# Optimization experiments

Hardware: AMD Instinct MI355X
Metric: run time of the kernel (lower is better)

## Reference

```python
import jax, jax.numpy as jnp
import numpy as np

B, S, D, H, T = 64, 512, 768, 384, 22  # batch, seq, bert dim, lstm hidden, tagset+2


def setup_inputs() -> dict:
    key = jax.random.key(0)
    ks = jax.random.split(key, 14)
    hidden_states = jax.random.normal(ks[0], (B, S, D), jnp.float32)
    # strictly increasing wordpiece start offsets, -1 padded (per-sample variable length)
    nw = np.array([S // 2 - (b % 16) * 4 for b in range(B)])  # number of valid start ids
    sid = -np.ones((B, S), np.int64)
    msk = np.zeros((B, S), np.int64)
    for b in range(B):
        sid[b, : nw[b]] = 1 + 2 * np.arange(nw[b])  # max = 2*nw-1 <= S-1
        msk[b, : nw[b] + 1] = 1  # word-level mask: nw+1 words incl. CLS slot
    start_ids = jnp.asarray(sid)
    masks = jnp.asarray(msk)
    sc = 0.05
    h0 = jax.random.normal(ks[1], (2, B, H), jnp.float32)
    c0 = jax.random.normal(ks[2], (2, B, H), jnp.float32)
    W_ih_f = jax.random.normal(ks[3], (4 * H, D), jnp.float32) * sc
    W_hh_f = jax.random.normal(ks[4], (4 * H, H), jnp.float32) * sc
    b_ih_f = jax.random.normal(ks[5], (4 * H,), jnp.float32) * sc
    b_hh_f = jax.random.normal(ks[6], (4 * H,), jnp.float32) * sc
    W_ih_b = jax.random.normal(ks[7], (4 * H, D), jnp.float32) * sc
    W_hh_b = jax.random.normal(ks[8], (4 * H, H), jnp.float32) * sc
    b_ih_b = jax.random.normal(ks[9], (4 * H,), jnp.float32) * sc
    b_hh_b = jax.random.normal(ks[10], (4 * H,), jnp.float32) * sc
    W_lin = jax.random.normal(ks[11], (T, 2 * H), jnp.float32) * sc
    b_lin = jax.random.normal(ks[12], (T,), jnp.float32) * sc
    return {"hidden_states": hidden_states, "h0": h0, "c0": c0,
            "W_ih_f": W_ih_f, "W_hh_f": W_hh_f, "b_ih_f": b_ih_f, "b_hh_f": b_hh_f,
            "W_ih_b": W_ih_b, "W_hh_b": W_hh_b, "b_ih_b": b_ih_b, "b_hh_b": b_hh_b,
            "W_lin": W_lin, "b_lin": b_lin, "start_ids": start_ids, "masks": masks}


def _lstm_dir(x, h0, c0, Wih, Whh, bih, bhh, reverse):
    # x: [B,S,D]; torch gate order i,f,g,o
    xg = jnp.einsum('bsd,gd->bsg', x, Wih) + bih + bhh  # [B,S,4H]
    xs = jnp.swapaxes(xg, 0, 1)  # [S,B,4H]
    if reverse:
        xs = xs[::-1]

    def step(carry, xt):
        h, c = carry
        g = xt + h @ Whh.T
        i, f, gg, o = jnp.split(g, 4, axis=-1)
        c = jax.nn.sigmoid(f) * c + jax.nn.sigmoid(i) * jnp.tanh(gg)
        h = jax.nn.sigmoid(o) * jnp.tanh(c)
        return (h, c), h

    _, hs = jax.lax.scan(step, (h0, c0), xs)
    if reverse:
        hs = hs[::-1]
    return jnp.swapaxes(hs, 0, 1)  # [B,S,H]


def _align(hidden_states, start_ids, masks):
    # word t embedding: t==0 -> token 0 (CLS); 1<=t<n -> token start_ids[t]-1
    # (last wordpiece of word t); t==n -> token start_ids[n-1]; else zero-pad.
    Bb, Ss, _ = hidden_states.shape
    t = jnp.arange(Ss)[None, :]
    valid = start_ids >= 0
    n = valid.sum(-1)  # [B] number of valid start ids
    last_sid = jnp.take_along_axis(start_ids, (n - 1)[:, None], axis=1)  # [B,1]
    idx = jnp.where(t == 0, 0,
          jnp.where(t < n[:, None], start_ids - 1,
          jnp.where(t == n[:, None], last_sid, 0)))
    idx = jnp.clip(idx, 0, Ss - 1)
    gathered = jnp.take_along_axis(hidden_states, idx[:, :, None], axis=1)
    sent_len = masks.sum(-1)  # word-level lengths (second loop in torch code)
    keep = (t < sent_len[:, None])[:, :, None]
    return jnp.where(keep, gathered, 0.0)


def reference(hidden_states, h0, c0, W_ih_f, W_hh_f, b_ih_f, b_hh_f,
              W_ih_b, W_hh_b, b_ih_b, b_hh_b, W_lin, b_lin, start_ids, masks):
    embeds = _align(hidden_states, start_ids, masks)  # q=1,k=0 => wordpiece-only
    hf = _lstm_dir(embeds, h0[0], c0[0], W_ih_f, W_hh_f, b_ih_f, b_hh_f, False)
    hb = _lstm_dir(embeds, h0[1], c0[1], W_ih_b, W_hh_b, b_ih_b, b_hh_b, True)
    lstm_out = jnp.concatenate([hf, hb], axis=-1)  # [B,S,2H]
    # dropout1 is identity in eval mode
    feats = lstm_out @ W_lin.T + b_lin  # [B,S,T]
    return feats
```

## Files before the change

### kernel.cpp

```cpp
#include <hip/hip_runtime.h>

typedef unsigned short u16;
typedef unsigned int u32;
typedef unsigned long long u64;

typedef short bf16x8 __attribute__((ext_vector_type(8)));
typedef float f32x4 __attribute__((ext_vector_type(4)));

#define NB 64
#define NS 512
#define ND 768
#define NH 384
#define NT_OUT 22
#define S2 272
#define NG 1536
#define MGEMM (NB*S2)

__device__ __forceinline__ u16 f2b(float f) {
    u32 u = __float_as_uint(f);
    u32 r = (u + 0x7fffu + ((u >> 16) & 1u)) >> 16;
    return (u16)r;
}
__device__ __forceinline__ float b2f(u16 s) { return __uint_as_float(((u32)s) << 16); }

__device__ __forceinline__ float sigm(float x) {
    return __builtin_amdgcn_rcpf(1.f + __expf(-x));
}
__device__ __forceinline__ float tanh_(float x) {
    return 1.f - 2.f * __builtin_amdgcn_rcpf(1.f + __expf(2.f * x));
}

__device__ __forceinline__ void gl_lds16(const void* g, void* l) {
    __builtin_amdgcn_global_load_lds(
        (const __attribute__((address_space(1))) unsigned int*)g,
        (__attribute__((address_space(3))) unsigned int*)l, 16, 0, 0);
}

__global__ void k_prep(const float* __restrict__ hidden, const int* __restrict__ start_ids,
                       const int* __restrict__ masks, u16* __restrict__ embeds) {
    int b = blockIdx.x >> 2;
    int quarter = blockIdx.x & 3;
    int tid = threadIdx.x;
    __shared__ int red[256];
    int cn = 0, cm = 0;
    for (int s = tid; s < NS; s += 256) {
        cn += (start_ids[b * NS + s] >= 0) ? 1 : 0;
        cm += (masks[b * NS + s] != 0) ? 1 : 0;
    }
    red[tid] = cn + (cm << 16);
    __syncthreads();
    #pragma unroll
    for (int off = 128; off > 0; off >>= 1) {
        if (tid < off) red[tid] += red[tid + off];
        __syncthreads();
    }
    int n = red[0] & 0xffff;
    int slen = red[0] >> 16;
    n = min(max(n, 1), NS);
    int last = start_ids[b * NS + n - 1];
    for (int t = quarter * 68; t < quarter * 68 + 68; ++t) {
        int idx;
        if (t == 0) idx = 0;
        else if (t < n) idx = start_ids[b * NS + t] - 1;
        else if (t == n) idx = last;
        else idx = 0;
        idx = min(max(idx, 0), NS - 1);
        bool keep = t < slen;
        const float* src = hidden + ((size_t)b * NS + idx) * ND;
        u16* dst = embeds + ((size_t)b * S2 + t) * ND;
        if (tid < 192) {
            float4 v = keep ? *(const float4*)(src + tid * 4) : make_float4(0.f, 0.f, 0.f, 0.f);
            union { u16 u[4]; uint2 q; } pk;
            pk.u[0] = f2b(v.x); pk.u[1] = f2b(v.y); pk.u[2] = f2b(v.z); pk.u[3] = f2b(v.w);
            *(uint2*)(dst + tid * 4) = pk.q;
        }
    }
}

__global__ void k_weights(const float* __restrict__ wf, const float* __restrict__ wb,
                          const float* __restrict__ bihf, const float* __restrict__ bhhf,
                          const float* __restrict__ bihb, const float* __restrict__ bhhb,
                          const float* __restrict__ h0,
                          u16* __restrict__ wihcat, float* __restrict__ biascat,
                          u16* __restrict__ h0buf) {
    int i0 = blockIdx.x * blockDim.x + threadIdx.x;
    int NTH = gridDim.x * blockDim.x;
    for (size_t i = i0; i < (size_t)2 * NG * ND; i += NTH) {
        size_t nrow = i / ND, k = i - nrow * ND;
        float v = (nrow < NG) ? wf[nrow * ND + k] : wb[(nrow - NG) * ND + k];
        wihcat[i] = f2b(v);
    }
    for (int i = i0; i < 2 * NG; i += NTH)
        biascat[i] = (i < NG) ? bihf[i] + bhhf[i] : bihb[i - NG] + bhhb[i - NG];
    for (int i = i0; i < 2 * NB * NH; i += NTH) h0buf[i] = f2b(h0[i]);
}

__global__ void k_packwhh(const float* __restrict__ whhf, const float* __restrict__ whhb,
                          u16* __restrict__ pack) {
    int ft = blockIdx.x * 256 + threadIdx.x;
    if (ft >= 2 * 4 * 4 * 6 * 12 * 64) return;
    int lane = ft & 63;
    int grp = ft >> 6;
    int ks = grp % 12; grp /= 12;
    int nt = grp % 6;  grp /= 6;
    int w  = grp & 3;  grp >>= 2;
    int qc = grp & 3;
    int d  = grp >> 2;
    const float* W = d ? whhb : whhf;
    int col = w * NH + qc * 96 + nt * 16 + (lane & 15);
    int k0 = ks * 32 + (lane >> 4) * 8;
    u16* dst = pack + (size_t)ft * 8;
    #pragma unroll
    for (int e = 0; e < 8; e++) dst[e] = f2b(W[(size_t)col * NH + k0 + e]);
}

__launch_bounds__(256, 2)
__global__ void k_gemm(const u16* __restrict__ A, const u16* __restrict__ Bw,
                       const float* __restrict__ biascat, u16* __restrict__ xg) {
    __shared__ u16 As[128 * 32];
    __shared__ u16 Bs[128 * 32];
    int tid = threadIdx.x;
    int lane = tid & 63, wid = tid >> 6;
    int l15 = lane & 15, q4 = lane >> 4;
    int bn = blockIdx.x;
    int bm = blockIdx.y;
    int wm = (wid >> 1) * 64, wn = (wid & 1) * 64;
    f32x4 acc[4][4] = {};
    for (int k0 = 0; k0 < ND; k0 += 32) {
        #pragma unroll
        for (int j = 0; j < 2; j++) {
            int fl = tid + j * 256;
            int row = fl >> 2, cb = fl & 3;
            const u16* ga = A + (size_t)(bm * 128 + row) * ND + k0 + cb * 8;
            gl_lds16(ga, &As[(size_t)(wid * 64 + j * 256) * 8]);
            const u16* gb = Bw + (size_t)(bn * 128 + row) * ND + k0 + cb * 8;
            gl_lds16(gb, &Bs[(size_t)(wid * 64 + j * 256) * 8]);
        }
        __syncthreads();
        bf16x8 af[4], bf[4];
        #pragma unroll
        for (int mt = 0; mt < 4; mt++)
            af[mt] = *(const bf16x8*)&As[(wm + mt * 16 + l15) * 32 + q4 * 8];
        #pragma unroll
        for (int nt = 0; nt < 4; nt++)
            bf[nt] = *(const bf16x8*)&Bs[(wn + nt * 16 + l15) * 32 + q4 * 8];
        #pragma unroll
        for (int mt = 0; mt < 4; mt++)
            #pragma unroll
            for (int nt = 0; nt < 4; nt++)
                acc[mt][nt] = __builtin_amdgcn_mfma_f32_16x16x32_bf16(af[mt], bf[nt], acc[mt][nt], 0, 0, 0);
        __syncthreads();
    }
    #pragma unroll
    for (int nt = 0; nt < 4; nt++) {
        int gn = bn * 128 + wn + nt * 16 + l15;
        int d = gn >= NG ? 1 : 0;
        int col = gn - d * NG;
        float bias = biascat[gn];
        #pragma unroll
        for (int mt = 0; mt < 4; mt++) {
            #pragma unroll
            for (int r = 0; r < 4; r++) {
                int m = bm * 128 + wm + mt * 16 + q4 * 4 + r;
                int b = m / S2, t = m - b * S2;
                float v = acc[mt][nt][r] + bias;
                xg[((size_t)(d * NB + b) * S2 + t) * NG + col] = f2b(v);
            }
        }
    }
}

__launch_bounds__(256, 1)
__global__ void k_recur(const u16* __restrict__ whhpack, const u16* __restrict__ xg,
                        const float* __restrict__ biascat, const u16* __restrict__ h0buf,
                        const float* __restrict__ c0, u16* __restrict__ hout,
                        int* __restrict__ flags) {
    int blk = blockIdx.x;
    int qc = blk >> 3;
    int cl = blk & 7;
    int d = cl >> 2;
    int g = cl & 3;
    int tid = threadIdx.x, lane = tid & 63, w = tid >> 6;
    int q4 = lane >> 4, l15 = lane & 15;

    __shared__ float preact[4][16 * 96];

    bf16x8 bfr[6][12];
    #pragma unroll
    for (int nt = 0; nt < 6; nt++)
        #pragma unroll
        for (int ks = 0; ks < 12; ks++)
            bfr[nt][ks] = *(const bf16x8*)(whhpack +
                ((size_t)((((d * 4 + qc) * 4 + w) * 6 + nt) * 12 + ks) * 64 + lane) * 8);

    int bb = tid / 12;
    int j0 = (tid % 12) * 8;
    float cre[8];
    if (tid < 192) {
        const float* cp = c0 + (size_t)(d * NB + g * 16 + bb) * NH + qc * 96 + j0;
        #pragma unroll
        for (int e = 0; e < 8; e++) cre[e] = cp[e];
    }
    float biasreg[6];
    #pragma unroll
    for (int nt = 0; nt < 6; nt++)
        biasreg[nt] = biascat[d * NG + w * NH + qc * 96 + nt * 16 + l15];

    int* flagp = flags + cl * NS;
    const u16* hd = hout + (size_t)d * NB * NS * NH;
    const u16* xgd = xg + (size_t)d * NB * S2 * NG;

    float ci[6][4];
    auto preload = [&](int it2) {
        int s2 = d ? (NS - 1 - it2) : it2;
        if (s2 < S2) {
            const u16* xrow = xgd + ((size_t)(g * 16) * S2 + s2) * NG + w * NH + qc * 96 + l15;
            #pragma unroll
            for (int nt = 0; nt < 6; nt++)
                #pragma unroll
                for (int r = 0; r < 4; r++)
                    ci[nt][r] = b2f(xrow[(size_t)(q4 * 4 + r) * S2 * NG + nt * 16]);
        } else {
            #pragma unroll
            for (int nt = 0; nt < 6; nt++)
                #pragma unroll
                for (int r = 0; r < 4; r++) ci[nt][r] = biasreg[nt];
        }
    };
    preload(0);

    int dep = 0;
    #pragma unroll 1
    for (int it = 0; it < NS; ++it) {
        int s = d ? (NS - 1 - it) : it;
        int tprev = d ? (s + 1) : (s - 1);

        bf16x8 af[12];
        if (it == 0) {
            const u16* hp = h0buf + (size_t)(d * NB + g * 16) * NH;
            #pragma unroll
            for (int ks = 0; ks < 12; ks++)
                af[ks] = *(const bf16x8*)(hp + (size_t)l15 * NH + ks * 32 + q4 * 8);
        } else {
            const u64* hp = (const u64*)(hd + ((size_t)(g * 16) * NS + tprev) * NH) + dep;
            #pragma unroll
            for (int ks = 0; ks < 12; ks++) {
                union { u64 q[2]; bf16x8 v; } u;
                const u64* p = hp + ((size_t)l15 * NS * NH + (size_t)ks * 32 + q4 * 8) / 4;
                u.q[0] = __hip_atomic_load(p,     __ATOMIC_RELAXED, __HIP_MEMORY_SCOPE_AGENT);
                u.q[1] = __hip_atomic_load(p + 1, __ATOMIC_RELAXED, __HIP_MEMORY_SCOPE_AGENT);
                af[ks] = u.v;
            }
        }

        f32x4 acc[6];
        #pragma unroll
        for (int nt = 0; nt < 6; nt++) {
            acc[nt][0] = ci[nt][0]; acc[nt][1] = ci[nt][1];
            acc[nt][2] = ci[nt][2]; acc[nt][3] = ci[nt][3];
        }
        #pragma unroll
        for (int ks = 0; ks < 12; ks++)
            #pragma unroll
            for (int nt = 0; nt < 6; nt++)
                acc[nt] = __builtin_amdgcn_mfma_f32_16x16x32_bf16(af[ks], bfr[nt][ks], acc[nt], 0, 0, 0);

        #pragma unroll
        for (int nt = 0; nt < 6; nt++)
            #pragma unroll
            for (int r = 0; r < 4; r++)
                preact[w][(q4 * 4 + r) * 96 + nt * 16 + l15] = acc[nt][r];
        __syncthreads();

        if (tid < 192) {
            int idx = bb * 96 + j0;
            u16* ho = hout + (((size_t)(d * NB + g * 16 + bb)) * NS + s) * NH + qc * 96 + j0;
            union { u16 u[8]; u64 q[2]; } pk;
            #pragma unroll
            for (int e = 0; e < 8; e++) {
                float gi = preact[0][idx + e], gf = preact[1][idx + e];
                float gg = preact[2][idx + e], go = preact[3][idx + e];
                float c = cre[e];
                float cn = sigm(gf) * c + sigm(gi) * tanh_(gg);
                float hn = sigm(go) * tanh_(cn);
                cre[e] = cn;
                pk.u[e] = f2b(hn);
            }
            __hip_atomic_store((u64*)ho,     pk.q[0], __ATOMIC_RELAXED, __HIP_MEMORY_SCOPE_AGENT);
            __hip_atomic_store((u64*)ho + 1, pk.q[1], __ATOMIC_RELAXED, __HIP_MEMORY_SCOPE_AGENT);
        }
        __syncthreads();

        if (tid == 0)
            __hip_atomic_fetch_add(&flagp[it], 1, __ATOMIC_RELAXED, __HIP_MEMORY_SCOPE_AGENT);

        if (it == NS - 1) break;

        preload(it + 1);

        int fv = 4;
        if (lane == 0) {
            while ((fv = __hip_atomic_load(&flagp[it], __ATOMIC_RELAXED, __HIP_MEMORY_SCOPE_AGENT)) < 4)
                __builtin_amdgcn_s_sleep(1);
        }
        fv = __shfl(fv, 0);
        dep = fv - 4;
    }
}

__global__ void k_final(const u16* __restrict__ hout, const float* __restrict__ wlin,
                        const float* __restrict__ blin, float* __restrict__ out) {
    int r = blockIdx.x * 256 + threadIdx.x;
    int b = r >> 9, t = r & 511;
    const u16* hf = hout + ((size_t)b * NS + t) * NH;
    const u16* hb = hout + ((size_t)(NB + b) * NS + t) * NH;
    float acc[NT_OUT];
    #pragma unroll
    for (int tt = 0; tt < NT_OUT; tt++) acc[tt] = blin[tt];
    #pragma unroll 1
    for (int half = 0; half < 2; half++) {
        const u16* hp = half ? hb : hf;
        #pragma unroll 1
        for (int k8 = 0; k8 < NH / 8; k8++) {
            uint4 pk = *(const uint4*)(hp + k8 * 8);
            float x[8];
            x[0] = __uint_as_float(pk.x << 16); x[1] = __uint_as_float(pk.x & 0xffff0000u);
            x[2] = __uint_as_float(pk.y << 16); x[3] = __uint_as_float(pk.y & 0xffff0000u);
            x[4] = __uint_as_float(pk.z << 16); x[5] = __uint_as_float(pk.z & 0xffff0000u);
            x[6] = __uint_as_float(pk.w << 16); x[7] = __uint_as_float(pk.w & 0xffff0000u);
            int kk = half * NH + k8 * 8;
            #pragma unroll
            for (int e = 0; e < 8; e++)
                #pragma unroll
                for (int tt = 0; tt < NT_OUT; tt++)
                    acc[tt] += x[e] * wlin[tt * (2 * NH) + kk + e];
        }
    }
    float* op = out + (size_t)r * NT_OUT;
    #pragma unroll
    for (int tt = 0; tt < NT_OUT; tt++) op[tt] = acc[tt];
}

extern "C" void kernel_launch(void* const* d_in, const int* in_sizes, int n_in,
                              void* d_out, int out_size, void* d_ws, size_t ws_size,
                              hipStream_t stream) {
    const float* hidden = (const float*)d_in[0];
    const float* h0     = (const float*)d_in[1];
    const float* c0     = (const float*)d_in[2];
    const float* Wihf   = (const float*)d_in[3];
    const float* Whhf   = (const float*)d_in[4];
    const float* bihf   = (const float*)d_in[5];
    const float* bhhf   = (const float*)d_in[6];
    const float* Wihb   = (const float*)d_in[7];
    const float* Whhb   = (const float*)d_in[8];
    const float* bihb   = (const float*)d_in[9];
    const float* bhhb   = (const float*)d_in[10];
    const float* Wlin   = (const float*)d_in[11];
    const float* blin   = (const float*)d_in[12];
    const int* start_ids = (const int*)d_in[13];
    const int* masks     = (const int*)d_in[14];
    float* out = (float*)d_out;

    char* ws = (char*)d_ws;
    size_t off = 0;
    auto alloc = [&](size_t bytes) { void* p = ws + off; off += (bytes + 255) & ~(size_t)255; return p; };
    u16* embeds   = (u16*)alloc((size_t)MGEMM * ND * 2);
    u16* wihcat   = (u16*)alloc((size_t)2 * NG * ND * 2);
    float* biascat = (float*)alloc((size_t)2 * NG * 4);
    u16* whhpack  = (u16*)alloc((size_t)2 * NG * NH * 2);
    u16* h0buf    = (u16*)alloc((size_t)2 * NB * NH * 2);
    u16* xg       = (u16*)alloc((size_t)2 * NB * S2 * NG * 2);
    u16* hout     = (u16*)alloc((size_t)2 * NB * NS * NH * 2);
    int* flags    = (int*)alloc((size_t)8 * NS * 4);

    (void)hipMemsetAsync(flags, 0, (size_t)8 * NS * 4, stream);
    k_prep<<<256, 256, 0, stream>>>(hidden, start_ids, masks, embeds);
    k_weights<<<512, 256, 0, stream>>>(Wihf, Wihb, bihf, bhhf, bihb, bhhb, h0,
                                       wihcat, biascat, h0buf);
    k_packwhh<<<576, 256, 0, stream>>>(Whhf, Whhb, whhpack);
    dim3 ggrid(2 * NG / 128, MGEMM / 128);
    k_gemm<<<ggrid, 256, 0, stream>>>(embeds, wihcat, biascat, xg);
    k_recur<<<32, 256, 0, stream>>>(whhpack, xg, biascat, h0buf, c0, hout, flags);
    k_final<<<128, 256, 0, stream>>>(hout, Wlin, blin, out);
}
```

Baseline: 3.051 ms.

## Replace per-step flag barrier with tagged h-exchange buffer and staggered partial MFMAs

The recurrence kernel no longer publishes h to the large hout array and then spins on a per-step counter flag. Each of the four cooperating blocks now writes its 96-column slice of h into a small triple-buffered exchange array, with the step number tagged into the low 16 bits of each word. Consumers poll those words directly, checking a sum of tags, and start MFMAs on their own slice (kept in LDS) before the peers' slices arrive, so the K loop is rotated per block. A startup handshake tests whether all four blocks of a cluster can see each other's writes with sc0 (non-coherent-L2-bypass) accesses and falls back to sc0 sc1 otherwise. This is meant to remove the flag round trip and the full barrier from the serial critical path, at the cost of inline asm cache-policy tricks and extra polling traffic.

```diff
diff --git a/kernel.cpp b/kernel.cpp
--- a/kernel.cpp
+++ b/kernel.cpp
@@ -6,6 +6,7 @@
 
 typedef short bf16x8 __attribute__((ext_vector_type(8)));
 typedef float f32x4 __attribute__((ext_vector_type(4)));
+typedef u32 u32x4 __attribute__((ext_vector_type(4)));
 
 #define NB 64
 #define NS 512
@@ -15,6 +16,7 @@
 #define S2 272
 #define NG 1536
 #define MGEMM (NB*S2)
+#define MAGIC 0x5A5AA5A5u
 
 __device__ __forceinline__ u16 f2b(float f) {
     u32 u = __float_as_uint(f);
@@ -34,6 +36,120 @@
     __builtin_amdgcn_global_load_lds(
         (const __attribute__((address_space(1))) unsigned int*)g,
         (__attribute__((address_space(3))) unsigned int*)l, 16, 0, 0);
+}
+
+__device__ __forceinline__ u32 ld_sc0(const int* p) {
+    u32 v;
+    asm volatile("global_load_dword %0, %1, off sc0 nt\n\t"
+                 "s_waitcnt vmcnt(0)"
+                 : "=&v"(v) : "v"(p) : "memory");
+    return v;
+}
+__device__ __forceinline__ u32 ld_sc01(const int* p) {
+    u32 v;
+    asm volatile("global_load_dword %0, %1, off sc0 sc1\n\t"
+                 "s_waitcnt vmcnt(0)"
+                 : "=&v"(v) : "v"(p) : "memory");
+    return v;
+}
+__device__ __forceinline__ void st_sc0(int* p, u32 v) {
+    asm volatile("global_store_dword %0, %1, off sc0" :: "v"(p), "v"(v) : "memory");
+}
+__device__ __forceinline__ void st_sc01(int* p, u32 v) {
+    asm volatile("global_store_dword %0, %1, off sc0 sc1" :: "v"(p), "v"(v) : "memory");
+}
+
+__device__ __forceinline__ void ld6_nw(bool fast, const u32* p,
+        u32x4& A, u32x4& B, u32x4& C, u32x4& D, u32x4& E, u32x4& F) {
+    if (fast)
+        asm volatile(
+            "global_load_dwordx4 %0, %6, off sc0 nt\n\t"
+            "global_load_dwordx4 %1, %6, off offset:16 sc0 nt\n\t"
+            "global_load_dwordx4 %2, %6, off offset:128 sc0 nt\n\t"
+            "global_load_dwordx4 %3, %6, off offset:144 sc0 nt\n\t"
+            "global_load_dwordx4 %4, %6, off offset:256 sc0 nt\n\t"
+            "global_load_dwordx4 %5, %6, off offset:272 sc0 nt"
+            : "=&v"(A), "=&v"(B), "=&v"(C), "=&v"(D), "=&v"(E), "=&v"(F)
+            : "v"(p) : "memory");
+    else
+        asm volatile(
+            "global_load_dwordx4 %0, %6, off sc0 sc1\n\t"
+            "global_load_dwordx4 %1, %6, off offset:16 sc0 sc1\n\t"
+            "global_load_dwordx4 %2, %6, off offset:128 sc0 sc1\n\t"
+            "global_load_dwordx4 %3, %6, off offset:144 sc0 sc1\n\t"
+            "global_load_dwordx4 %4, %6, off offset:256 sc0 sc1\n\t"
+            "global_load_dwordx4 %5, %6, off offset:272 sc0 sc1"
+            : "=&v"(A), "=&v"(B), "=&v"(C), "=&v"(D), "=&v"(E), "=&v"(F)
+            : "v"(p) : "memory");
+}
+__device__ __forceinline__ void ld6_wt(bool fast, const u32* p,
+        u32x4& A, u32x4& B, u32x4& C, u32x4& D, u32x4& E, u32x4& F) {
+    if (fast)
+        asm volatile(
+            "global_load_dwordx4 %0, %6, off sc0 nt\n\t"
+            "global_load_dwordx4 %1, %6, off offset:16 sc0 nt\n\t"
+            "global_load_dwordx4 %2, %6, off offset:128 sc0 nt\n\t"
+            "global_load_dwordx4 %3, %6, off offset:144 sc0 nt\n\t"
+            "global_load_dwordx4 %4, %6, off offset:256 sc0 nt\n\t"
+            "global_load_dwordx4 %5, %6, off offset:272 sc0 nt\n\t"
+            "s_waitcnt vmcnt(0)"
+            : "=&v"(A), "=&v"(B), "=&v"(C), "=&v"(D), "=&v"(E), "=&v"(F)
+            : "v"(p) : "memory");
+    else
+        asm volatile(
+            "global_load_dwordx4 %0, %6, off sc0 sc1\n\t"
+            "global_load_dwordx4 %1, %6, off offset:16 sc0 sc1\n\t"
+            "global_load_dwordx4 %2, %6, off offset:128 sc0 sc1\n\t"
+            "global_load_dwordx4 %3, %6, off offset:144 sc0 sc1\n\t"
+            "global_load_dwordx4 %4, %6, off offset:256 sc0 sc1\n\t"
+            "global_load_dwordx4 %5, %6, off offset:272 sc0 sc1\n\t"
+            "s_waitcnt vmcnt(0)"
+            : "=&v"(A), "=&v"(B), "=&v"(C), "=&v"(D), "=&v"(E), "=&v"(F)
+            : "v"(p) : "memory");
+}
+__device__ __forceinline__ void st8(bool fast, u32* p, u32x4 lo, u32x4 hi) {
+    if (fast)
+        asm volatile("global_store_dwordx4 %0, %1, off sc0\n\t"
+                     "global_store_dwordx4 %0, %2, off offset:16 sc0"
+                     :: "v"(p), "v"(lo), "v"(hi) : "memory");
+    else
+        asm volatile("global_store_dwordx4 %0, %1, off sc0 sc1\n\t"
+                     "global_store_dwordx4 %0, %2, off offset:16 sc0 sc1"
+                     :: "v"(p), "v"(lo), "v"(hi) : "memory");
+}
+__device__ __forceinline__ void wait_vm6() {
+    __builtin_amdgcn_sched_barrier(0);
+    asm volatile("s_waitcnt vmcnt(6)" ::: "memory");
+    __builtin_amdgcn_sched_barrier(0);
+}
+__device__ __forceinline__ void wait_vm0() {
+    __builtin_amdgcn_sched_barrier(0);
+    asm volatile("s_waitcnt vmcnt(0)" ::: "memory");
+    __builtin_amdgcn_sched_barrier(0);
+}
+__device__ __forceinline__ void ldsbar() {
+    asm volatile("s_waitcnt lgkmcnt(0)" ::: "memory");
+    __builtin_amdgcn_s_barrier();
+    __builtin_amdgcn_sched_barrier(0);
+}
+
+__device__ __forceinline__ u32 sum6(const u32x4& a, const u32x4& b, const u32x4& c,
+                                    const u32x4& d, const u32x4& e, const u32x4& f) {
+    u32 s = (a[0] & 0xffffu) + (a[1] & 0xffffu) + (a[2] & 0xffffu) + (a[3] & 0xffffu);
+    s += (b[0] & 0xffffu) + (b[1] & 0xffffu) + (b[2] & 0xffffu) + (b[3] & 0xffffu);
+    s += (c[0] & 0xffffu) + (c[1] & 0xffffu) + (c[2] & 0xffffu) + (c[3] & 0xffffu);
+    s += (d[0] & 0xffffu) + (d[1] & 0xffffu) + (d[2] & 0xffffu) + (d[3] & 0xffffu);
+    s += (e[0] & 0xffffu) + (e[1] & 0xffffu) + (e[2] & 0xffffu) + (e[3] & 0xffffu);
+    s += (f[0] & 0xffffu) + (f[1] & 0xffffu) + (f[2] & 0xffffu) + (f[3] & 0xffffu);
+    return s;
+}
+__device__ __forceinline__ bf16x8 packf(const u32x4& lo, const u32x4& hi) {
+    union { u32 q[4]; bf16x8 v; } U;
+    U.q[0] = __builtin_amdgcn_perm(lo[1], lo[0], 0x07060302u);
+    U.q[1] = __builtin_amdgcn_perm(lo[3], lo[2], 0x07060302u);
+    U.q[2] = __builtin_amdgcn_perm(hi[1], hi[0], 0x07060302u);
+    U.q[3] = __builtin_amdgcn_perm(hi[3], hi[2], 0x07060302u);
+    return U.v;
 }
 
 __global__ void k_prep(const float* __restrict__ hidden, const int* __restrict__ start_ids,
@@ -174,27 +290,31 @@
 __global__ void k_recur(const u16* __restrict__ whhpack, const u16* __restrict__ xg,
                         const float* __restrict__ biascat, const u16* __restrict__ h0buf,
                         const float* __restrict__ c0, u16* __restrict__ hout,
-                        int* __restrict__ flags) {
-    int blk = blockIdx.x;
-    int qc = blk >> 3;
-    int cl = blk & 7;
-    int d = cl >> 2;
-    int g = cl & 3;
-    int tid = threadIdx.x, lane = tid & 63, w = tid >> 6;
-    int q4 = lane >> 4, l15 = lane & 15;
+                        int* __restrict__ flags, u32* __restrict__ xch) {
+    const int blk = blockIdx.x;
+    const int qc = blk >> 3;
+    const int cl = blk & 7;
+    const int d = cl >> 2;
+    const int g = cl & 3;
+    const int tid = threadIdx.x, lane = tid & 63, w = tid >> 6;
+    const int q4 = lane >> 4, l15 = lane & 15;
 
     __shared__ float preact[4][16 * 96];
+    __shared__ u16 hlds[16 * 104];
+    __shared__ int s_fast;
 
     bf16x8 bfr[6][12];
     #pragma unroll
     for (int nt = 0; nt < 6; nt++)
         #pragma unroll
-        for (int ks = 0; ks < 12; ks++)
-            bfr[nt][ks] = *(const bf16x8*)(whhpack +
-                ((size_t)((((d * 4 + qc) * 4 + w) * 6 + nt) * 12 + ks) * 64 + lane) * 8);
-
-    int bb = tid / 12;
-    int j0 = (tid % 12) * 8;
+        for (int j = 0; j < 12; j++) {
+            int ksg = ((qc + (j / 3)) & 3) * 3 + (j % 3);
+            bfr[nt][j] = *(const bf16x8*)(whhpack +
+                ((size_t)((((d * 4 + qc) * 4 + w) * 6 + nt) * 12 + ksg) * 64 + lane) * 8);
+        }
+
+    const int bb = tid / 12;
+    const int j0 = (tid % 12) * 8;
     float cre[8];
     if (tid < 192) {
         const float* cp = c0 + (size_t)(d * NB + g * 16 + bb) * NH + qc * 96 + j0;
@@ -206,8 +326,30 @@
     for (int nt = 0; nt < 6; nt++)
         biasreg[nt] = biascat[d * NG + w * NH + qc * 96 + nt * 16 + l15];
 
-    int* flagp = flags + cl * NS;
-    const u16* hd = hout + (size_t)d * NB * NS * NH;
+    if (tid == 0) {
+        int* pzb = flags + cl * 64;
+        int* pmb = flags + 2048 + cl * 64;
+        st_sc0(pzb + qc * 16, MAGIC);
+        u32 seen = 1u << qc;
+        for (int spin = 0; spin < 512 && seen != 0xFu; ++spin) {
+            #pragma unroll
+            for (int r = 0; r < 4; ++r)
+                if (!((seen >> r) & 1u) && ld_sc0(pzb + r * 16) == MAGIC) seen |= 1u << r;
+            __builtin_amdgcn_s_sleep(2);
+        }
+        st_sc01(pmb + qc * 16, (int)(0x100u | seen));
+        u32 m = 0xFu;
+        #pragma unroll
+        for (int r = 0; r < 4; ++r) {
+            u32 v;
+            do { v = ld_sc01(pmb + r * 16); } while (!(v & 0x100u));
+            m &= v;
+        }
+        s_fast = ((m & 0xFu) == 0xFu) ? 1 : 0;
+    }
+    __syncthreads();
+    const bool fast = (s_fast != 0);
+
     const u16* xgd = xg + (size_t)d * NB * S2 * NG;
 
     float ci[6][4];
@@ -229,53 +371,111 @@
     };
     preload(0);
 
-    int dep = 0;
     #pragma unroll 1
     for (int it = 0; it < NS; ++it) {
         int s = d ? (NS - 1 - it) : it;
-        int tprev = d ? (s + 1) : (s - 1);
-
-        bf16x8 af[12];
+        f32x4 acc[6];
+
         if (it == 0) {
+            bf16x8 af0[12];
             const u16* hp = h0buf + (size_t)(d * NB + g * 16) * NH;
             #pragma unroll
-            for (int ks = 0; ks < 12; ks++)
-                af[ks] = *(const bf16x8*)(hp + (size_t)l15 * NH + ks * 32 + q4 * 8);
+            for (int j = 0; j < 12; j++) {
+                int ksg = ((qc + (j / 3)) & 3) * 3 + (j % 3);
+                af0[j] = *(const bf16x8*)(hp + (size_t)l15 * NH + ksg * 32 + q4 * 8);
+            }
+            #pragma unroll
+            for (int nt = 0; nt < 6; nt++) {
+                acc[nt][0] = ci[nt][0]; acc[nt][1] = ci[nt][1];
+                acc[nt][2] = ci[nt][2]; acc[nt][3] = ci[nt][3];
+            }
+            preload(1);
+            #pragma unroll
+            for (int j = 0; j < 12; j++)
+                #pragma unroll
+                for (int nt = 0; nt < 6; nt++)
+                    acc[nt] = __builtin_amdgcn_mfma_f32_16x16x32_bf16(af0[j], bfr[nt][j], acc[nt], 0, 0, 0);
         } else {
-            const u64* hp = (const u64*)(hd + ((size_t)(g * 16) * NS + tprev) * NH) + dep;
-            #pragma unroll
-            for (int ks = 0; ks < 12; ks++) {
-                union { u64 q[2]; bf16x8 v; } u;
-                const u64* p = hp + ((size_t)l15 * NS * NH + (size_t)ks * 32 + q4 * 8) / 4;
-                u.q[0] = __hip_atomic_load(p,     __ATOMIC_RELAXED, __HIP_MEMORY_SCOPE_AGENT);
-                u.q[1] = __hip_atomic_load(p + 1, __ATOMIC_RELAXED, __HIP_MEMORY_SCOPE_AGENT);
-                af[ks] = u.v;
+            bf16x8 afo0 = *(const bf16x8*)&hlds[l15 * 104 + 0 * 32 + q4 * 8];
+            bf16x8 afo1 = *(const bf16x8*)&hlds[l15 * 104 + 1 * 32 + q4 * 8];
+            bf16x8 afo2 = *(const bf16x8*)&hlds[l15 * 104 + 2 * 32 + q4 * 8];
+            const u32 T = (u32)it;
+            const u32 want = T * 24u;
+            u32* xrow = xch + (((size_t)(T % 3u) * 8 + cl) * 16 + l15) * 384 + q4 * 8;
+            u32* pA = xrow + ((qc + 1) & 3) * 96;
+            u32* pB = xrow + ((qc + 2) & 3) * 96;
+            u32* pC = xrow + ((qc + 3) & 3) * 96;
+            u32x4 a0, a1, a2, a3, a4, a5, b0, b1, b2, b3, b4, b5, e0, e1, e2, e3, e4, e5;
+            ld6_nw(fast, pA, a0, a1, a2, a3, a4, a5);
+            ld6_nw(fast, pB, b0, b1, b2, b3, b4, b5);
+            #pragma unroll
+            for (int nt = 0; nt < 6; nt++) {
+                acc[nt][0] = ci[nt][0]; acc[nt][1] = ci[nt][1];
+                acc[nt][2] = ci[nt][2]; acc[nt][3] = ci[nt][3];
             }
-        }
-
-        f32x4 acc[6];
-        #pragma unroll
-        for (int nt = 0; nt < 6; nt++) {
-            acc[nt][0] = ci[nt][0]; acc[nt][1] = ci[nt][1];
-            acc[nt][2] = ci[nt][2]; acc[nt][3] = ci[nt][3];
-        }
-        #pragma unroll
-        for (int ks = 0; ks < 12; ks++)
-            #pragma unroll
-            for (int nt = 0; nt < 6; nt++)
-                acc[nt] = __builtin_amdgcn_mfma_f32_16x16x32_bf16(af[ks], bfr[nt][ks], acc[nt], 0, 0, 0);
+            #pragma unroll
+            for (int nt = 0; nt < 6; nt++)
+                acc[nt] = __builtin_amdgcn_mfma_f32_16x16x32_bf16(afo0, bfr[nt][0], acc[nt], 0, 0, 0);
+            #pragma unroll
+            for (int nt = 0; nt < 6; nt++)
+                acc[nt] = __builtin_amdgcn_mfma_f32_16x16x32_bf16(afo1, bfr[nt][1], acc[nt], 0, 0, 0);
+            #pragma unroll
+            for (int nt = 0; nt < 6; nt++)
+                acc[nt] = __builtin_amdgcn_mfma_f32_16x16x32_bf16(afo2, bfr[nt][2], acc[nt], 0, 0, 0);
+            wait_vm6();
+            while (!__all(sum6(a0, a1, a2, a3, a4, a5) == want))
+                ld6_wt(fast, pA, a0, a1, a2, a3, a4, a5);
+            bf16x8 afA0 = packf(a0, a1), afA1 = packf(a2, a3), afA2 = packf(a4, a5);
+            ld6_nw(fast, pC, e0, e1, e2, e3, e4, e5);
+            #pragma unroll
+            for (int nt = 0; nt < 6; nt++)
+                acc[nt] = __builtin_amdgcn_mfma_f32_16x16x32_bf16(afA0, bfr[nt][3], acc[nt], 0, 0, 0);
+            #pragma unroll
+            for (int nt = 0; nt < 6; nt++)
+                acc[nt] = __builtin_amdgcn_mfma_f32_16x16x32_bf16(afA1, bfr[nt][4], acc[nt], 0, 0, 0);
+            #pragma unroll
+            for (int nt = 0; nt < 6; nt++)
+                acc[nt] = __builtin_amdgcn_mfma_f32_16x16x32_bf16(afA2, bfr[nt][5], acc[nt], 0, 0, 0);
+            wait_vm6();
+            while (!__all(sum6(b0, b1, b2, b3, b4, b5) == want))
+                ld6_wt(fast, pB, b0, b1, b2, b3, b4, b5);
+            bf16x8 afB0 = packf(b0, b1), afB1 = packf(b2, b3), afB2 = packf(b4, b5);
+            #pragma unroll
+            for (int nt = 0; nt < 6; nt++)
+                acc[nt] = __builtin_amdgcn_mfma_f32_16x16x32_bf16(afB0, bfr[nt][6], acc[nt], 0, 0, 0);
+            #pragma unroll
+            for (int nt = 0; nt < 6; nt++)
+                acc[nt] = __builtin_amdgcn_mfma_f32_16x16x32_bf16(afB1, bfr[nt][7], acc[nt], 0, 0, 0);
+            #pragma unroll
+            for (int nt = 0; nt < 6; nt++)
+                acc[nt] = __builtin_amdgcn_mfma_f32_16x16x32_bf16(afB2, bfr[nt][8], acc[nt], 0, 0, 0);
+            wait_vm0();
+            while (!__all(sum6(e0, e1, e2, e3, e4, e5) == want))
+                ld6_wt(fast, pC, e0, e1, e2, e3, e4, e5);
+            bf16x8 afC0 = packf(e0, e1), afC1 = packf(e2, e3), afC2 = packf(e4, e5);
+            if (it + 1 < NS) preload(it + 1);
+            #pragma unroll
+            for (int nt = 0; nt < 6; nt++)
+                acc[nt] = __builtin_amdgcn_mfma_f32_16x16x32_bf16(afC0, bfr[nt][9], acc[nt], 0, 0, 0);
+            #pragma unroll
+            for (int nt = 0; nt < 6; nt++)
+                acc[nt] = __builtin_amdgcn_mfma_f32_16x16x32_bf16(afC1, bfr[nt][10], acc[nt], 0, 0, 0);
+            #pragma unroll
+            for (int nt = 0; nt < 6; nt++)
+                acc[nt] = __builtin_amdgcn_mfma_f32_16x16x32_bf16(afC2, bfr[nt][11], acc[nt], 0, 0, 0);
+        }
 
         #pragma unroll
         for (int nt = 0; nt < 6; nt++)
             #pragma unroll
             for (int r = 0; r < 4; r++)
                 preact[w][(q4 * 4 + r) * 96 + nt * 16 + l15] = acc[nt][r];
-        __syncthreads();
+        ldsbar();
 
         if (tid < 192) {
             int idx = bb * 96 + j0;
             u16* ho = hout + (((size_t)(d * NB + g * 16 + bb)) * NS + s) * NH + qc * 96 + j0;
-            union { u16 u[8]; u64 q[2]; } pk;
+            union { u16 u[8]; u32x4 v4; } pk;
             #pragma unroll
             for (int e = 0; e < 8; e++) {
                 float gi = preact[0][idx + e], gf = preact[1][idx + e];
@@ -286,25 +486,18 @@
                 cre[e] = cn;
                 pk.u[e] = f2b(hn);
             }
-            __hip_atomic_store((u64*)ho,     pk.q[0], __ATOMIC_RELAXED, __HIP_MEMORY_SCOPE_AGENT);
-            __hip_atomic_store((u64*)ho + 1, pk.q[1], __ATOMIC_RELAXED, __HIP_MEMORY_SCOPE_AGENT);
-        }
-        __syncthreads();
-
-        if (tid == 0)
-            __hip_atomic_fetch_add(&flagp[it], 1, __ATOMIC_RELAXED, __HIP_MEMORY_SCOPE_AGENT);
-
-        if (it == NS - 1) break;
-
-        preload(it + 1);
-
-        int fv = 4;
-        if (lane == 0) {
-            while ((fv = __hip_atomic_load(&flagp[it], __ATOMIC_RELAXED, __HIP_MEMORY_SCOPE_AGENT)) < 4)
-                __builtin_amdgcn_s_sleep(1);
-        }
-        fv = __shfl(fv, 0);
-        dep = fv - 4;
+            *(u32x4*)ho = pk.v4;
+            *(u32x4*)&hlds[bb * 104 + j0] = pk.v4;
+            u32 t2 = (u32)it + 1u;
+            u32x4 lo, hi;
+            lo[0] = ((u32)pk.u[0] << 16) | t2; lo[1] = ((u32)pk.u[1] << 16) | t2;
+            lo[2] = ((u32)pk.u[2] << 16) | t2; lo[3] = ((u32)pk.u[3] << 16) | t2;
+            hi[0] = ((u32)pk.u[4] << 16) | t2; hi[1] = ((u32)pk.u[5] << 16) | t2;
+            hi[2] = ((u32)pk.u[6] << 16) | t2; hi[3] = ((u32)pk.u[7] << 16) | t2;
+            u32* xp = xch + (((size_t)(t2 % 3u) * 8 + cl) * 16 + bb) * 384 + qc * 96 + j0;
+            st8(fast, xp, lo, hi);
+        }
+        ldsbar();
     }
 }
 
@@ -372,14 +565,16 @@
     u16* xg       = (u16*)alloc((size_t)2 * NB * S2 * NG * 2);
     u16* hout     = (u16*)alloc((size_t)2 * NB * NS * NH * 2);
     int* flags    = (int*)alloc((size_t)8 * NS * 4);
+    u32* xch      = (u32*)alloc((size_t)3 * 8 * 16 * 384 * 4);
 
     (void)hipMemsetAsync(flags, 0, (size_t)8 * NS * 4, stream);
+    (void)hipMemsetAsync(xch, 0, (size_t)3 * 8 * 16 * 384 * 4, stream);
     k_prep<<<256, 256, 0, stream>>>(hidden, start_ids, masks, embeds);
     k_weights<<<512, 256, 0, stream>>>(Wihf, Wihb, bihf, bhhf, bihb, bhhb, h0,
                                        wihcat, biascat, h0buf);
     k_packwhh<<<576, 256, 0, stream>>>(Whhf, Whhb, whhpack);
     dim3 ggrid(2 * NG / 128, MGEMM / 128);
     k_gemm<<<ggrid, 256, 0, stream>>>(embeds, wihcat, biascat, xg);
-    k_recur<<<32, 256, 0, stream>>>(whhpack, xg, biascat, h0buf, c0, hout, flags);
+    k_recur<<<32, 256, 0, stream>>>(whhpack, xg, biascat, h0buf, c0, hout, flags, xch);
     k_final<<<128, 256, 0, stream>>>(hout, Wlin, blin, out);
 }
```

Measured after the change: 2.577 ms. 15.5% less time.
